# Kernel optimization log

Measured on AMD Instinct MI355X. Metric: run time of the kernel, lower is better.

Reference implementation:

```python
import jax, jax.numpy as jnp
import numpy as np

D_MODEL = 1024
E_MODEL = 2
D_STATE = 16
D_CONV = 4
D_IN = E_MODEL * D_MODEL            # 2048
DT_RANK = int(np.ceil(D_MODEL / 16))  # 64
B_SZ, SEQ = 1, 2048


def setup_inputs() -> dict:
    key = jax.random.key(0)
    ks = jax.random.split(key, 9)
    s = lambda fan: 1.0 / np.sqrt(fan)
    return {
        "x": jax.random.normal(ks[0], (B_SZ, SEQ, D_MODEL), jnp.float32),
        "W_in": jax.random.normal(ks[1], (D_MODEL, 2 * D_IN), jnp.float32) * s(D_MODEL),
        "conv_w": jax.random.normal(ks[2], (D_CONV, D_IN), jnp.float32) * s(D_CONV),
        "conv_b": jnp.zeros((D_IN,), jnp.float32),
        "W_x": jax.random.normal(ks[3], (D_IN, DT_RANK + 2 * D_STATE), jnp.float32) * s(D_IN),
        "W_dt": jax.random.normal(ks[4], (DT_RANK, D_IN), jnp.float32) * s(DT_RANK),
        "b_dt": jax.random.normal(ks[5], (D_IN,), jnp.float32) * 0.01,
        "D": jnp.ones((D_IN,), jnp.float32),
        "W_out": jax.random.normal(ks[6], (D_IN, D_MODEL), jnp.float32) * s(D_IN),
    }


def _causal_depthwise_conv(x, w, b):
    # x: (b, l, d_in); w: (d_conv, d_in) depthwise taps; causal left pad
    L = x.shape[1]
    xp = jnp.pad(x, ((0, 0), (D_CONV - 1, 0), (0, 0)))
    y = b
    for k in range(D_CONV):  # small fixed kernel width
        y = y + xp[:, k:k + L, :] * w[k]
    return y


def _selective_scan(u, delta, A, Bm, Cm, D):
    # u, delta: (b,l,d); A: (d,n); Bm, Cm: (b,l,n); D: (d,)
    dA = jnp.einsum('bld,dn->bldn', delta, A)
    dB_u = jnp.einsum('bld,bld,bln->bldn', delta, u, Bm)
    # replicate tf.pad(dA[:,1:], [[0,0],[1,1],[0,0],[0,0]])[:,1:]
    t = jnp.pad(dA[:, 1:], ((0, 0), (1, 1), (0, 0), (0, 0)))[:, 1:]
    t = jnp.flip(t, axis=1)
    t = jnp.cumsum(t, axis=1)
    dA_cs = jnp.flip(jnp.exp(t), axis=1)
    xs = jnp.cumsum(dB_u * dA_cs, axis=1) / (dA_cs + 1e-12)
    y = jnp.einsum('bldn,bln->bld', xs, Cm)
    return y + u * D


def reference(x, W_in, conv_w, conv_b, W_x, W_dt, b_dt, D, W_out):
    seq_len = x.shape[1]
    x_and_res = x @ W_in                                  # (b,l,2*d_in)
    xi, res = jnp.split(x_and_res, [D_IN], axis=-1)
    xi = _causal_depthwise_conv(xi, conv_w, conv_b)[:, :seq_len, :]
    xi = jax.nn.swish(xi)
    # SSM
    A = -jnp.exp(jnp.log(jnp.arange(1, D_STATE + 1, dtype=jnp.float32)))  # (n,)
    A = jnp.broadcast_to(A, (D_IN, D_STATE))
    x_dbl = xi @ W_x                                      # (b,l,dtr+2n)
    delta, Bm, Cm = jnp.split(x_dbl, [DT_RANK, DT_RANK + D_STATE], axis=-1)
    delta = jax.nn.softplus(delta @ W_dt + b_dt)          # (b,l,d_in)
    y = _selective_scan(xi, delta, A, Bm, Cm, D)
    y = y * jax.nn.swish(res)
    return y @ W_out
```

## Files before the change

### kernel.cpp

```cpp
#include <hip/hip_runtime.h>
#include <hip/hip_bf16.h>

#define L_SEQ 2048
#define DMODEL 1024
#define DIN 2048
#define DTR 64
#define NST 16
#define CCH 128
#define CHL 16

typedef unsigned short u16;
typedef __bf16 bf16x8 __attribute__((ext_vector_type(8)));
typedef float f32x4 __attribute__((ext_vector_type(4)));

__device__ inline u16 f2bf(float v) {
    __bf16 h = (__bf16)v;
    return __builtin_bit_cast(unsigned short, h);
}
__device__ inline float rcpf(float x) { return __builtin_amdgcn_rcpf(x); }
__device__ inline float swishf(float v) { return v * rcpf(1.f + __expf(-v)); }
__device__ inline float softplusf(float v) {
    return (v > 20.f) ? v : __logf(1.f + __expf(v));
}

__device__ inline void powers16(float v, float* p) {
    p[0] = v;
    p[1] = v * v;
    p[2] = p[1] * v;
    p[3] = p[1] * p[1];
    p[4] = p[3] * p[0];  p[5] = p[3] * p[1];  p[6] = p[3] * p[2];  p[7] = p[3] * p[3];
    p[8] = p[7] * p[0];  p[9] = p[7] * p[1];  p[10] = p[7] * p[2]; p[11] = p[7] * p[3];
    p[12] = p[7] * p[4]; p[13] = p[7] * p[5]; p[14] = p[7] * p[6]; p[15] = p[7] * p[7];
}

__device__ inline float* lqp(float* wsf, int idx) {
    return wsf + ((idx >> 11) << 12) + (idx & 2047);
}

template<int TBN, bool SP>
__global__ __launch_bounds__(256) void gemm_bf16(const u16* __restrict__ A,
                                                 const u16* __restrict__ Bt,
                                                 float* __restrict__ C,
                                                 const float* __restrict__ bias,
                                                 int M, int N, int K) {
    constexpr int LDSZ = (128 + TBN) * 64;
    constexpr int ROUNDS = (128 + TBN) / 32;
    constexpr int FN = TBN / 32;
    __shared__ u16 smem[2 * LDSZ];

    const int tid = threadIdx.x;
    const int lane = tid & 63;
    const int wid = tid >> 6;
    const int wm = wid >> 1;
    const int wn = wid & 1;
    const int bm = blockIdx.y * 128;
    const int bn = blockIdx.x * TBN;

    const int srow8 = lane >> 3;
    const int schunk = lane & 7;
    const int lm = lane & 15;
    const int lk = lane >> 4;

    f32x4 acc[4][FN];
#pragma unroll
    for (int i = 0; i < 4; ++i)
#pragma unroll
        for (int j = 0; j < FN; ++j) acc[i][j] = (f32x4){0.f, 0.f, 0.f, 0.f};

    auto stage = [&](int buf, int t) {
        const int k0 = t * 64;
        u16* base = smem + buf * LDSZ;
#pragma unroll
        for (int rr = 0; rr < ROUNDS; ++rr) {
            int row = rr * 32 + wid * 8;
            int grow = row + srow8;
            const u16* src;
            if (row < 128) src = A + (size_t)(bm + grow) * K + k0 + schunk * 8;
            else           src = Bt + (size_t)(bn + grow - 128) * K + k0 + schunk * 8;
            u16* dst = base + row * 64;
            __builtin_amdgcn_global_load_lds(
                (const __attribute__((address_space(1))) void*)src,
                (__attribute__((address_space(3))) void*)dst, 16, 0, 0);
        }
    };

    auto compute = [&](int buf) {
        const u16* base = smem + buf * LDSZ;
#pragma unroll
        for (int kk = 0; kk < 2; ++kk) {
            bf16x8 av[4], bv[FN];
#pragma unroll
            for (int fm = 0; fm < 4; ++fm)
                av[fm] = *(const bf16x8*)(base + (wm * 64 + fm * 16 + lm) * 64 + kk * 32 + lk * 8);
#pragma unroll
            for (int fn = 0; fn < FN; ++fn)
                bv[fn] = *(const bf16x8*)(base + (128 + wn * (TBN / 2) + fn * 16 + lm) * 64 + kk * 32 + lk * 8);
#pragma unroll
            for (int fm = 0; fm < 4; ++fm)
#pragma unroll
                for (int fn = 0; fn < FN; ++fn)
                    acc[fm][fn] = __builtin_amdgcn_mfma_f32_16x16x32_bf16(av[fm], bv[fn], acc[fm][fn], 0, 0, 0);
        }
    };

    const int nt = K / 64;
    int cur = 0;
    stage(0, 0);
    __syncthreads();
    for (int t = 0; t < nt - 1; ++t) {
        stage(cur ^ 1, t + 1);
        compute(cur);
        __syncthreads();
        cur ^= 1;
    }
    compute(cur);

#pragma unroll
    for (int fm = 0; fm < 4; ++fm) {
#pragma unroll
        for (int fn = 0; fn < FN; ++fn) {
            int col = bn + wn * (TBN / 2) + fn * 16 + lm;
#pragma unroll
            for (int j = 0; j < 4; ++j) {
                int row = bm + wm * 64 + fm * 16 + lk * 4 + j;
                float v = acc[fm][fn][j];
                if (SP) {
                    v += bias[col];
                    v = softplusf(v);
                }
                C[(size_t)row * N + col] = v;
            }
        }
    }
}

__global__ __launch_bounds__(256) void gemm_bf16_sk(const u16* __restrict__ A, int lda,
                                                    const u16* __restrict__ Bt, int ldb,
                                                    float* __restrict__ P,
                                                    int M, int N, int K, int kc) {
    constexpr int TBN = 32;
    constexpr int LDSZ = (128 + TBN) * 64;
    constexpr int ROUNDS = (128 + TBN) / 32;
    __shared__ u16 smem[2 * LDSZ];

    const int tid = threadIdx.x;
    const int lane = tid & 63;
    const int wid = tid >> 6;
    const int wm = wid >> 1;
    const int wn = wid & 1;
    const int bm = blockIdx.y * 128;
    const int bn = blockIdx.x * TBN;
    const int kbeg = blockIdx.z * kc;
    float* Cz = P + (size_t)blockIdx.z * M * N;

    const int srow8 = lane >> 3;
    const int schunk = lane & 7;
    const int lm = lane & 15;
    const int lk = lane >> 4;

    f32x4 acc[4];
#pragma unroll
    for (int i = 0; i < 4; ++i) acc[i] = (f32x4){0.f, 0.f, 0.f, 0.f};

    auto stage = [&](int buf, int t) {
        const int k0 = kbeg + t * 64;
        u16* base = smem + buf * LDSZ;
#pragma unroll
        for (int rr = 0; rr < ROUNDS; ++rr) {
            int row = rr * 32 + wid * 8;
            int grow = row + srow8;
            const u16* src;
            if (row < 128) src = A + (size_t)(bm + grow) * lda + k0 + schunk * 8;
            else           src = Bt + (size_t)(bn + grow - 128) * ldb + k0 + schunk * 8;
            u16* dst = base + row * 64;
            __builtin_amdgcn_global_load_lds(
                (const __attribute__((address_space(1))) void*)src,
                (__attribute__((address_space(3))) void*)dst, 16, 0, 0);
        }
    };

    auto compute = [&](int buf) {
        const u16* base = smem + buf * LDSZ;
#pragma unroll
        for (int kk = 0; kk < 2; ++kk) {
            bf16x8 av[4], bv;
#pragma unroll
            for (int fm = 0; fm < 4; ++fm)
                av[fm] = *(const bf16x8*)(base + (wm * 64 + fm * 16 + lm) * 64 + kk * 32 + lk * 8);
            bv = *(const bf16x8*)(base + (128 + wn * 16 + lm) * 64 + kk * 32 + lk * 8);
#pragma unroll
            for (int fm = 0; fm < 4; ++fm)
                acc[fm] = __builtin_amdgcn_mfma_f32_16x16x32_bf16(av[fm], bv, acc[fm], 0, 0, 0);
        }
    };

    const int nt = kc / 64;
    int cur = 0;
    stage(0, 0);
    __syncthreads();
    for (int t = 0; t < nt - 1; ++t) {
        stage(cur ^ 1, t + 1);
        compute(cur);
        __syncthreads();
        cur ^= 1;
    }
    compute(cur);

#pragma unroll
    for (int fm = 0; fm < 4; ++fm) {
        int col = bn + wn * 16 + lm;
#pragma unroll
        for (int j = 0; j < 4; ++j) {
            int row = bm + wm * 64 + fm * 16 + lk * 4 + j;
            Cz[(size_t)row * N + col] = acc[fm][j];
        }
    }
}

__global__ __launch_bounds__(256) void cast_bf16_vec4(const float* __restrict__ in,
                                                      u16* __restrict__ out, int nvec) {
    int i = blockIdx.x * 256 + threadIdx.x;
    if (i >= nvec) return;
    float4 v = ((const float4*)in)[i];
    ushort4 o;
    o.x = f2bf(v.x); o.y = f2bf(v.y); o.z = f2bf(v.z); o.w = f2bf(v.w);
    ((ushort4*)out)[i] = o;
}

__global__ __launch_bounds__(256) void castT_bf16(const float* __restrict__ W,
                                                  u16* __restrict__ Wt, int K, int N) {
    __shared__ u16 tile[64][65];
    int n0 = blockIdx.x * 64, k0 = blockIdx.y * 64;
    int tn = threadIdx.x & 63, t4 = threadIdx.x >> 6;
#pragma unroll
    for (int j = 0; j < 16; ++j) {
        int k = t4 + j * 4;
        if (n0 + tn < N) tile[tn][k] = f2bf(W[(size_t)(k0 + k) * N + n0 + tn]);
    }
    __syncthreads();
#pragma unroll
    for (int j = 0; j < 16; ++j) {
        int n = t4 + j * 4;
        if (n0 + n < N) Wt[(size_t)(n0 + n) * K + k0 + tn] = tile[n][tn];
    }
}

__global__ __launch_bounds__(256) void cast_xd(const float* __restrict__ xdbl,
                                               u16* __restrict__ xd) {
    int id = blockIdx.x * 256 + threadIdx.x;
    int l = id >> 6, k = id & 63;
    xd[id] = f2bf(xdbl[l * 96 + k]);
}

__global__ __launch_bounds__(256) void reduce_sk(const float* __restrict__ P,
                                                 float* __restrict__ xdbl) {
    int i = blockIdx.x * 256 + threadIdx.x;
    float s = 0.f;
#pragma unroll
    for (int z = 0; z < 8; ++z) s += P[z * (L_SEQ * 96) + i];
    xdbl[i] = s;
}

__global__ __launch_bounds__(256) void conv_swish(const float* __restrict__ xr,
                                                  const float* __restrict__ cw,
                                                  const float* __restrict__ cb,
                                                  float* __restrict__ xi,
                                                  u16* __restrict__ xib) {
    int id = blockIdx.x * 256 + threadIdx.x;
    int l = id >> 11;
    int d = id & (DIN - 1);
    float acc = cb[d];
#pragma unroll
    for (int k = 0; k < 4; ++k) {
        int ls = l - 3 + k;
        if (ls >= 0) acc += xr[ls * 4096 + d] * cw[k * DIN + d];
    }
    float sw = swishf(acc);
    xi[id] = sw;
    xib[id] = f2bf(sw);
}

__global__ __launch_bounds__(256) void scanA(const float* __restrict__ delta,
                                             const float* __restrict__ u,
                                             const float* __restrict__ xdbl,
                                             float* __restrict__ wsf,
                                             float* __restrict__ csum) {
    __shared__ float sh[CHL][16];
    const int tid = threadIdx.x;
    const int c = blockIdx.y;
    const int d = blockIdx.x * 256 + tid;
    const int l0 = c * CHL;
    {
        int l = tid >> 4, j = tid & 15;
        sh[l][j] = xdbl[(l0 + l) * 96 + DTR + j];
    }
    __syncthreads();
    float q[16];
#pragma unroll
    for (int n = 0; n < 16; ++n) q[n] = 0.f;
    float s = 0.f;
#pragma unroll 2
    for (int l = 0; l < CHL; ++l) {
        float dl = delta[(l0 + l) * DIN + d];
        float ul = u[(l0 + l) * DIN + d];
        float bb[16];
        const float4* shv = (const float4*)&sh[l][0];
        *(float4*)&bb[0] = shv[0];  *(float4*)&bb[4] = shv[1];
        *(float4*)&bb[8] = shv[2];  *(float4*)&bb[12] = shv[3];
        float v = __expf(-dl);
        float p[16];
        powers16(v, p);
        float dlul = dl * ul;
#pragma unroll
        for (int n = 0; n < 16; ++n) q[n] = q[n] * p[n] + dlul * bb[n];
        s += dl;
    }
    float* dst = lqp(wsf, (c * DIN + d) * 16);
    *(float4*)(dst + 0)  = make_float4(q[0], q[1], q[2], q[3]);
    *(float4*)(dst + 4)  = make_float4(q[4], q[5], q[6], q[7]);
    *(float4*)(dst + 8)  = make_float4(q[8], q[9], q[10], q[11]);
    *(float4*)(dst + 12) = make_float4(q[12], q[13], q[14], q[15]);
    csum[c * DIN + d] = s;
}

__global__ __launch_bounds__(256) void scanB(float* __restrict__ wsf,
                                             const float* __restrict__ csum,
                                             float* __restrict__ send) {
    int gid = blockIdx.x * 256 + threadIdx.x;
    int n = gid & 15;
    int d = gid >> 4;
    const float An = -(float)(n + 1);
    float q = 0.f;
#pragma unroll 4
    for (int c = 0; c < CCH; ++c) {
        float cs = csum[c * DIN + d];
        float w = __expf(An * cs);
        float* lq = lqp(wsf, (c * DIN + d) * 16 + n);
        float lv = *lq;
        *lq = q;
        q = q * w + lv;
    }
    if (n == 0) {
        double ssum = 0.0;
        for (int c = CCH - 1; c >= 0; --c) {
            ssum += (double)csum[c * DIN + d];
            send[c * DIN + d] = (float)ssum;
        }
    }
}

__global__ __launch_bounds__(256) void scanC(const float* __restrict__ delta,
                                             float* __restrict__ u,
                                             const float* __restrict__ xdbl,
                                             float* __restrict__ wsf,
                                             const float* __restrict__ send,
                                             const float* __restrict__ Dvec,
                                             const float* __restrict__ xr) {
    __shared__ float sh[CHL][32];
    const int tid = threadIdx.x;
    const int c = blockIdx.y;
    const int d = blockIdx.x * 256 + tid;
    const int l0 = c * CHL;
#pragma unroll
    for (int k = 0; k < 2; ++k) {
        int idx = tid + k * 256;
        int l = idx >> 5, j = idx & 31;
        sh[l][j] = xdbl[(l0 + l) * 96 + DTR + j];
    }
    __syncthreads();
    float q[16];
    {
        const float* src = lqp(wsf, (c * DIN + d) * 16);
        float4 t0 = *(const float4*)(src + 0);
        float4 t1 = *(const float4*)(src + 4);
        float4 t2 = *(const float4*)(src + 8);
        float4 t3 = *(const float4*)(src + 12);
        q[0] = t0.x; q[1] = t0.y; q[2] = t0.z; q[3] = t0.w;
        q[4] = t1.x; q[5] = t1.y; q[6] = t1.z; q[7] = t1.w;
        q[8] = t2.x; q[9] = t2.y; q[10] = t2.z; q[11] = t2.w;
        q[12] = t3.x; q[13] = t3.y; q[14] = t3.z; q[15] = t3.w;
    }
    const float send_cd = send[c * DIN + d];
    const float Dd = Dvec[d];
    float s = 0.f;
#pragma unroll 2
    for (int l = 0; l < CHL; ++l) {
        float dl = delta[(l0 + l) * DIN + d];
        float ul = u[(l0 + l) * DIN + d];
        float bb[32];
        const float4* shv = (const float4*)&sh[l][0];
        *(float4*)&bb[0]  = shv[0]; *(float4*)&bb[4]  = shv[1];
        *(float4*)&bb[8]  = shv[2]; *(float4*)&bb[12] = shv[3];
        *(float4*)&bb[16] = shv[4]; *(float4*)&bb[20] = shv[5];
        *(float4*)&bb[24] = shv[6]; *(float4*)&bb[28] = shv[7];
        float v = __expf(-dl);
        float p[16];
        powers16(v, p);
        float dlul = dl * ul;
#pragma unroll
        for (int n = 0; n < 16; ++n) q[n] = q[n] * p[n] + dlul * bb[n];
        s += dl;
        float suf = send_cd - s;
        float contrib;
        float ac[4] = {0.f, 0.f, 0.f, 0.f};
        if (suf < 0.8f) {
#pragma unroll
            for (int n = 0; n < 16; ++n) ac[n & 3] += q[n] * bb[16 + n];
            contrib = (ac[0] + ac[1]) + (ac[2] + ac[3]);
        } else {
            float w = __expf(-suf);
            float e[16];
            powers16(w, e);
            if (suf > 40.f) {
#pragma unroll
                for (int n = 0; n < 16; ++n) ac[n & 3] += (q[n] * e[n]) * bb[16 + n];
                contrib = ((ac[0] + ac[1]) + (ac[2] + ac[3])) * 1e12f;
            } else {
#pragma unroll
                for (int n = 0; n < 16; ++n) {
                    float g = e[n] * rcpf(e[n] + 1e-12f);
                    ac[n & 3] += (q[n] * g) * bb[16 + n];
                }
                contrib = (ac[0] + ac[1]) + (ac[2] + ac[3]);
            }
        }
        float y = contrib + ul * Dd;
        float r = xr[(l0 + l) * 4096 + DIN + d];
        u[(l0 + l) * DIN + d] = y * swishf(r);
    }
}

extern "C" void kernel_launch(void* const* d_in, const int* in_sizes, int n_in,
                              void* d_out, int out_size, void* d_ws, size_t ws_size,
                              hipStream_t stream) {
    const float* x      = (const float*)d_in[0];
    const float* W_in   = (const float*)d_in[1];
    const float* conv_w = (const float*)d_in[2];
    const float* conv_b = (const float*)d_in[3];
    const float* W_x    = (const float*)d_in[4];
    const float* W_dt   = (const float*)d_in[5];
    const float* b_dt   = (const float*)d_in[6];
    const float* Dvec   = (const float*)d_in[7];
    const float* W_out  = (const float*)d_in[8];
    float* out = (float*)d_out;

    float* ws = (float*)d_ws;
    float* xr    = ws;
    float* xi    = ws + 8388608;
    float* xdbl  = ws + 12582912;
    float* csum  = ws + 16973824;
    float* send  = ws + 17235968;
    float* WxTf  = ws + 17498112;

    u16* x_bf   = (u16*)(ws + 12779520);
    u16* WinT   = (u16*)(ws + 13828096);
    u16* xi_bf  = (u16*)(ws + 12779520);
    float* Psk  = ws + 14876672;
    float* delta= ws + 12779520;
    (void)delta;

    float* deltaR = ws + 12779520;

    float* delta_buf = ws + 12779520;

    u16* xd_bf  = (u16*)(ws + 16973824);
    u16* WdtT   = (u16*)(ws + 17039360);
    u16* WxT    = (u16*)WxTf;
    u16* y_bf   = (u16*)ws;
    u16* WoutT  = (u16*)(ws + 2097152);

    cast_bf16_vec4<<<2048, 256, 0, stream>>>(x, x_bf, (L_SEQ * DMODEL) / 4);
    castT_bf16<<<dim3(4096 / 64, 1024 / 64), 256, 0, stream>>>(W_in, WinT, DMODEL, 4096);
    gemm_bf16<128, false><<<dim3(4096 / 128, L_SEQ / 128), 256, 0, stream>>>(
        x_bf, WinT, xr, nullptr, L_SEQ, 4096, DMODEL);
    conv_swish<<<(L_SEQ * DIN) / 256, 256, 0, stream>>>(xr, conv_w, conv_b, xi, xi_bf);
    castT_bf16<<<dim3(2, 2048 / 64), 256, 0, stream>>>(W_x, WxT, DIN, 96);
    gemm_bf16_sk<<<dim3(3, L_SEQ / 128, 8), 256, 0, stream>>>(
        xi_bf, DIN, WxT, DIN, Psk, L_SEQ, 96, DIN, 256);
    reduce_sk<<<(L_SEQ * 96) / 256, 256, 0, stream>>>(Psk, xdbl);
    cast_xd<<<(L_SEQ * DTR) / 256, 256, 0, stream>>>(xdbl, xd_bf);
    castT_bf16<<<dim3(2048 / 64, 64 / 64), 256, 0, stream>>>(W_dt, WdtT, DTR, DIN);
    gemm_bf16<128, true><<<dim3(DIN / 128, L_SEQ / 128), 256, 0, stream>>>(
        xd_bf, WdtT, delta_buf, b_dt, L_SEQ, DIN, DTR);
    scanA<<<dim3(DIN / 256, CCH), 256, 0, stream>>>(delta_buf, xi, xdbl, ws, csum);
    scanB<<<(DIN * NST) / 256, 256, 0, stream>>>(ws, csum, send);
    scanC<<<dim3(DIN / 256, CCH), 256, 0, stream>>>(delta_buf, xi, xdbl, ws, send, Dvec, xr);
    cast_bf16_vec4<<<4096, 256, 0, stream>>>(xi, y_bf, (L_SEQ * DIN) / 4);
    castT_bf16<<<dim3(1024 / 64, 2048 / 64), 256, 0, stream>>>(W_out, WoutT, DIN, DMODEL);
    gemm_bf16<64, false><<<dim3(DMODEL / 64, L_SEQ / 128), 256, 0, stream>>>(
        y_bf, WoutT, out, nullptr, L_SEQ, DMODEL, DIN);
}
```

Baseline: 188.5 us.

## Fuse input and weight casts into one prep kernel and fold bf16 casts into producers

All the fp32-to-bf16 casts of x and the transposed weight casts are merged into a single prep kernel, replacing five separate launches. The bf16 cast of the dt slice moves into reduce_sk, and the bf16 output cast moves into scanC, which removes the cast_xd and final cast_bf16_vec4 kernels and the fp32 y round trip. The workspace layout is also redone so buffers no longer alias, and the odd lqp interleaved addressing becomes a plain contiguous layout. The cost is a larger workspace footprint.

```diff
diff --git a/kernel.cpp b/kernel.cpp
--- a/kernel.cpp
+++ b/kernel.cpp
@@ -31,10 +31,6 @@
     p[4] = p[3] * p[0];  p[5] = p[3] * p[1];  p[6] = p[3] * p[2];  p[7] = p[3] * p[3];
     p[8] = p[7] * p[0];  p[9] = p[7] * p[1];  p[10] = p[7] * p[2]; p[11] = p[7] * p[3];
     p[12] = p[7] * p[4]; p[13] = p[7] * p[5]; p[14] = p[7] * p[6]; p[15] = p[7] * p[7];
-}
-
-__device__ inline float* lqp(float* wsf, int idx) {
-    return wsf + ((idx >> 11) << 12) + (idx & 2047);
 }
 
 template<int TBN, bool SP>
@@ -217,20 +213,10 @@
     }
 }
 
-__global__ __launch_bounds__(256) void cast_bf16_vec4(const float* __restrict__ in,
-                                                      u16* __restrict__ out, int nvec) {
-    int i = blockIdx.x * 256 + threadIdx.x;
-    if (i >= nvec) return;
-    float4 v = ((const float4*)in)[i];
-    ushort4 o;
-    o.x = f2bf(v.x); o.y = f2bf(v.y); o.z = f2bf(v.z); o.w = f2bf(v.w);
-    ((ushort4*)out)[i] = o;
-}
-
-__global__ __launch_bounds__(256) void castT_bf16(const float* __restrict__ W,
-                                                  u16* __restrict__ Wt, int K, int N) {
+__device__ inline void castT_dev(const float* __restrict__ W, u16* __restrict__ Wt,
+                                 int K, int N, int bx, int by) {
     __shared__ u16 tile[64][65];
-    int n0 = blockIdx.x * 64, k0 = blockIdx.y * 64;
+    int n0 = bx * 64, k0 = by * 64;
     int tn = threadIdx.x & 63, t4 = threadIdx.x >> 6;
 #pragma unroll
     for (int j = 0; j < 16; ++j) {
@@ -245,20 +231,48 @@
     }
 }
 
-__global__ __launch_bounds__(256) void cast_xd(const float* __restrict__ xdbl,
-                                               u16* __restrict__ xd) {
-    int id = blockIdx.x * 256 + threadIdx.x;
-    int l = id >> 6, k = id & 63;
-    xd[id] = f2bf(xdbl[l * 96 + k]);
+__global__ __launch_bounds__(256) void prep_fused(const float* __restrict__ x,
+                                                  const float* __restrict__ W_in,
+                                                  const float* __restrict__ W_x,
+                                                  const float* __restrict__ W_dt,
+                                                  const float* __restrict__ W_out,
+                                                  u16* __restrict__ xbf,
+                                                  u16* __restrict__ WinT,
+                                                  u16* __restrict__ WxT,
+                                                  u16* __restrict__ WdtT,
+                                                  u16* __restrict__ WoutT) {
+    int b = blockIdx.x;
+    if (b < 2048) {
+        int i = b * 256 + threadIdx.x;
+        float4 v = ((const float4*)x)[i];
+        ushort4 o;
+        o.x = f2bf(v.x); o.y = f2bf(v.y); o.z = f2bf(v.z); o.w = f2bf(v.w);
+        ((ushort4*)xbf)[i] = o;
+    } else if (b < 3072) {
+        int t = b - 2048;
+        castT_dev(W_in, WinT, DMODEL, 4096, t & 63, t >> 6);
+    } else if (b < 3136) {
+        int t = b - 3072;
+        castT_dev(W_x, WxT, DIN, 96, t & 1, t >> 1);
+    } else if (b < 3168) {
+        int t = b - 3136;
+        castT_dev(W_dt, WdtT, DTR, DIN, t, 0);
+    } else {
+        int t = b - 3168;
+        castT_dev(W_out, WoutT, DIN, DMODEL, t & 15, t >> 4);
+    }
 }
 
 __global__ __launch_bounds__(256) void reduce_sk(const float* __restrict__ P,
-                                                 float* __restrict__ xdbl) {
+                                                 float* __restrict__ xdbl,
+                                                 u16* __restrict__ xdbf) {
     int i = blockIdx.x * 256 + threadIdx.x;
     float s = 0.f;
 #pragma unroll
     for (int z = 0; z < 8; ++z) s += P[z * (L_SEQ * 96) + i];
     xdbl[i] = s;
+    int l = i / 96, k = i - l * 96;
+    if (k < DTR) xdbf[l * DTR + k] = f2bf(s);
 }
 
 __global__ __launch_bounds__(256) void conv_swish(const float* __restrict__ xr,
@@ -283,7 +297,7 @@
 __global__ __launch_bounds__(256) void scanA(const float* __restrict__ delta,
                                              const float* __restrict__ u,
                                              const float* __restrict__ xdbl,
-                                             float* __restrict__ wsf,
+                                             float* __restrict__ localQ,
                                              float* __restrict__ csum) {
     __shared__ float sh[CHL][16];
     const int tid = threadIdx.x;
@@ -315,7 +329,7 @@
         for (int n = 0; n < 16; ++n) q[n] = q[n] * p[n] + dlul * bb[n];
         s += dl;
     }
-    float* dst = lqp(wsf, (c * DIN + d) * 16);
+    float* dst = localQ + (size_t)(c * DIN + d) * 16;
     *(float4*)(dst + 0)  = make_float4(q[0], q[1], q[2], q[3]);
     *(float4*)(dst + 4)  = make_float4(q[4], q[5], q[6], q[7]);
     *(float4*)(dst + 8)  = make_float4(q[8], q[9], q[10], q[11]);
@@ -323,7 +337,7 @@
     csum[c * DIN + d] = s;
 }
 
-__global__ __launch_bounds__(256) void scanB(float* __restrict__ wsf,
+__global__ __launch_bounds__(256) void scanB(float* __restrict__ localQ,
                                              const float* __restrict__ csum,
                                              float* __restrict__ send) {
     int gid = blockIdx.x * 256 + threadIdx.x;
@@ -335,7 +349,7 @@
     for (int c = 0; c < CCH; ++c) {
         float cs = csum[c * DIN + d];
         float w = __expf(An * cs);
-        float* lq = lqp(wsf, (c * DIN + d) * 16 + n);
+        float* lq = localQ + (size_t)(c * DIN + d) * 16 + n;
         float lv = *lq;
         *lq = q;
         q = q * w + lv;
@@ -350,12 +364,13 @@
 }
 
 __global__ __launch_bounds__(256) void scanC(const float* __restrict__ delta,
-                                             float* __restrict__ u,
+                                             const float* __restrict__ u,
                                              const float* __restrict__ xdbl,
-                                             float* __restrict__ wsf,
+                                             const float* __restrict__ localQ,
                                              const float* __restrict__ send,
                                              const float* __restrict__ Dvec,
-                                             const float* __restrict__ xr) {
+                                             const float* __restrict__ xr,
+                                             u16* __restrict__ ybf) {
     __shared__ float sh[CHL][32];
     const int tid = threadIdx.x;
     const int c = blockIdx.y;
@@ -370,7 +385,7 @@
     __syncthreads();
     float q[16];
     {
-        const float* src = lqp(wsf, (c * DIN + d) * 16);
+        const float* src = localQ + (size_t)(c * DIN + d) * 16;
         float4 t0 = *(const float4*)(src + 0);
         float4 t1 = *(const float4*)(src + 4);
         float4 t2 = *(const float4*)(src + 8);
@@ -426,7 +441,7 @@
         }
         float y = contrib + ul * Dd;
         float r = xr[(l0 + l) * 4096 + DIN + d];
-        u[(l0 + l) * DIN + d] = y * swishf(r);
+        ybf[(l0 + l) * DIN + d] = f2bf(y * swishf(r));
     }
 }
 
@@ -445,48 +460,37 @@
     float* out = (float*)d_out;
 
     float* ws = (float*)d_ws;
-    float* xr    = ws;
-    float* xi    = ws + 8388608;
-    float* xdbl  = ws + 12582912;
-    float* csum  = ws + 16973824;
-    float* send  = ws + 17235968;
-    float* WxTf  = ws + 17498112;
-
-    u16* x_bf   = (u16*)(ws + 12779520);
-    u16* WinT   = (u16*)(ws + 13828096);
-    u16* xi_bf  = (u16*)(ws + 12779520);
-    float* Psk  = ws + 14876672;
-    float* delta= ws + 12779520;
-    (void)delta;
-
-    float* deltaR = ws + 12779520;
-
-    float* delta_buf = ws + 12779520;
-
-    u16* xd_bf  = (u16*)(ws + 16973824);
-    u16* WdtT   = (u16*)(ws + 17039360);
-    u16* WxT    = (u16*)WxTf;
-    u16* y_bf   = (u16*)ws;
-    u16* WoutT  = (u16*)(ws + 2097152);
-
-    cast_bf16_vec4<<<2048, 256, 0, stream>>>(x, x_bf, (L_SEQ * DMODEL) / 4);
-    castT_bf16<<<dim3(4096 / 64, 1024 / 64), 256, 0, stream>>>(W_in, WinT, DMODEL, 4096);
+    float* xr     = ws;
+    float* xi     = ws + 8388608;
+    u16*   xibf   = (u16*)(ws + 12582912);
+    float* xdbl   = ws + 14680064;
+    float* delta  = ws + 14876672;
+    float* localQ = ws + 19070976;
+    float* csum   = ws + 23265280;
+    float* send   = ws + 23527424;
+    u16*   xbf    = (u16*)(ws + 23789568);
+    u16*   WinT   = (u16*)(ws + 24838144);
+    u16*   WxT    = (u16*)(ws + 26935296);
+    u16*   WdtT   = (u16*)(ws + 27033600);
+    u16*   WoutT  = (u16*)(ws + 27099136);
+    u16*   xdbf   = (u16*)(ws + 28147712);
+    float* Psk    = ws + 28213248;
+    u16*   ybf    = (u16*)(ws + 29786112);
+
+    prep_fused<<<3680, 256, 0, stream>>>(x, W_in, W_x, W_dt, W_out,
+                                         xbf, WinT, WxT, WdtT, WoutT);
     gemm_bf16<128, false><<<dim3(4096 / 128, L_SEQ / 128), 256, 0, stream>>>(
-        x_bf, WinT, xr, nullptr, L_SEQ, 4096, DMODEL);
-    conv_swish<<<(L_SEQ * DIN) / 256, 256, 0, stream>>>(xr, conv_w, conv_b, xi, xi_bf);
-    castT_bf16<<<dim3(2, 2048 / 64), 256, 0, stream>>>(W_x, WxT, DIN, 96);
+        xbf, WinT, xr, nullptr, L_SEQ, 4096, DMODEL);
+    conv_swish<<<(L_SEQ * DIN) / 256, 256, 0, stream>>>(xr, conv_w, conv_b, xi, xibf);
     gemm_bf16_sk<<<dim3(3, L_SEQ / 128, 8), 256, 0, stream>>>(
-        xi_bf, DIN, WxT, DIN, Psk, L_SEQ, 96, DIN, 256);
-    reduce_sk<<<(L_SEQ * 96) / 256, 256, 0, stream>>>(Psk, xdbl);
-    cast_xd<<<(L_SEQ * DTR) / 256, 256, 0, stream>>>(xdbl, xd_bf);
-    castT_bf16<<<dim3(2048 / 64, 64 / 64), 256, 0, stream>>>(W_dt, WdtT, DTR, DIN);
+        xibf, DIN, WxT, DIN, Psk, L_SEQ, 96, DIN, 256);
+    reduce_sk<<<(L_SEQ * 96) / 256, 256, 0, stream>>>(Psk, xdbl, xdbf);
     gemm_bf16<128, true><<<dim3(DIN / 128, L_SEQ / 128), 256, 0, stream>>>(
-        xd_bf, WdtT, delta_buf, b_dt, L_SEQ, DIN, DTR);
-    scanA<<<dim3(DIN / 256, CCH), 256, 0, stream>>>(delta_buf, xi, xdbl, ws, csum);
-    scanB<<<(DIN * NST) / 256, 256, 0, stream>>>(ws, csum, send);
-    scanC<<<dim3(DIN / 256, CCH), 256, 0, stream>>>(delta_buf, xi, xdbl, ws, send, Dvec, xr);
-    cast_bf16_vec4<<<4096, 256, 0, stream>>>(xi, y_bf, (L_SEQ * DIN) / 4);
-    castT_bf16<<<dim3(1024 / 64, 2048 / 64), 256, 0, stream>>>(W_out, WoutT, DIN, DMODEL);
+        xdbf, WdtT, delta, b_dt, L_SEQ, DIN, DTR);
+    scanA<<<dim3(DIN / 256, CCH), 256, 0, stream>>>(delta, xi, xdbl, localQ, csum);
+    scanB<<<(DIN * NST) / 256, 256, 0, stream>>>(localQ, csum, send);
+    scanC<<<dim3(DIN / 256, CCH), 256, 0, stream>>>(delta, xi, xdbl, localQ, send,
+                                                    Dvec, xr, ybf);
     gemm_bf16<64, false><<<dim3(DMODEL / 64, L_SEQ / 128), 256, 0, stream>>>(
-        y_bf, WoutT, out, nullptr, L_SEQ, DMODEL, DIN);
-}
+        ybf, WoutT, out, nullptr, L_SEQ, DMODEL, DIN);
+}
```

Result: faster. 162.5 us (-13.8%).
